# Optimization experiments

Measured on AMD Instinct MI355X. Metric: run time of the kernel, lower is better.

## Reference

```python
import jax, jax.numpy as jnp
import numpy as np

VOL = 64          # self.vol_size
SPACE = 0.2       # space_size (cubic), space_center = 0
IMG = 255.0       # normalization constant in the source (2*u/255 - 1)


def setup_inputs() -> dict:
    key = jax.random.key(0)
    ks = jax.random.split(key, 5)
    B, V, C, Hf, Wf = 2, 4, 32, 64, 64
    features = jax.random.normal(ks[0], (B, V, C, Hf, Wf), jnp.float32)
    # near-identity rotations, cameras ~0.5m away, focal ~200, principal point 128
    camera_R = jnp.eye(3, dtype=jnp.float32)[None, None] + 0.01 * jax.random.normal(ks[1], (B, V, 3, 3), jnp.float32)
    camera_T = jnp.array([0.0, 0.0, 0.5], jnp.float32) + 0.01 * jax.random.normal(ks[2], (B, V, 3), jnp.float32)
    K0 = jnp.array([[200.0, 0.0, 128.0], [0.0, 200.0, 128.0], [0.0, 0.0, 1.0]], jnp.float32)
    Kmask = jnp.array([[1.0, 0.0, 1.0], [0.0, 1.0, 1.0], [0.0, 0.0, 0.0]], jnp.float32)
    camera_K = K0[None, None] + 0.5 * jax.random.normal(ks[3], (B, V, 3, 3), jnp.float32) * Kmask
    root_world = 0.01 * jax.random.normal(ks[4], (B, 3), jnp.float32)
    return dict(features=features, camera_R=camera_R, camera_T=camera_T,
                camera_K=camera_K, root_world=root_world)


def _bilinear_sample(feat, x, y):
    """PyTorch F.grid_sample, mode=bilinear, padding=zeros, align_corners=False.
    feat: [N,C,H,W]; x,y: [N,P] pixel-space coords (already unnormalized).
    Returns [N,C,P]."""
    N, C, H, W = feat.shape
    x0 = jnp.floor(x); y0 = jnp.floor(y)
    x1 = x0 + 1.0;     y1 = y0 + 1.0
    wx1 = x - x0; wx0 = 1.0 - wx1
    wy1 = y - y0; wy0 = 1.0 - wy1
    feat_flat = feat.reshape(N, C, H * W)

    def gather(xi, yi, w):
        valid = (xi >= 0) & (xi <= W - 1) & (yi >= 0) & (yi <= H - 1)
        xi_c = jnp.clip(xi, 0, W - 1).astype(jnp.int32)
        yi_c = jnp.clip(yi, 0, H - 1).astype(jnp.int32)
        idx = yi_c * W + xi_c                                   # [N,P]
        vals = jnp.take_along_axis(feat_flat, idx[:, None, :], axis=2)  # [N,C,P]
        return vals * (w * valid.astype(feat.dtype))[:, None, :]

    return (gather(x0, y0, wx0 * wy0) + gather(x1, y0, wx1 * wy0)
            + gather(x0, y1, wx0 * wy1) + gather(x1, y1, wx1 * wy1))


def reference(features, camera_R, camera_T, camera_K, root_world):
    B, V, C, Hf, Wf = features.shape
    D = VOL
    # _build_grid: 64^3 points, xyz order, spanning SPACE around center 0
    r = jnp.arange(D, dtype=jnp.float32)
    z, y, x = jnp.meshgrid(r, r, r, indexing='ij')
    grid = jnp.stack([x, y, z], axis=0) / (D - 1)               # [3,D,D,D]
    pts = ((grid - 0.5) * SPACE).reshape(3, -1).T               # [P,3], P = D^3
    # relative camera translation: new_T = R @ root + T
    new_T = jnp.einsum('bvij,bj->bvi', camera_R, root_world) + camera_T
    # project: pts_cam = pts @ R^T + T  -> [B,V,P,3]
    pts_cam = jnp.einsum('pj,bvij->bvpi', pts, camera_R) + new_T[:, :, None, :]
    zc = jnp.maximum(pts_cam[..., 2], 1e-5)
    fx = camera_K[:, :, 0, 0][..., None]; fy = camera_K[:, :, 1, 1][..., None]
    cx = camera_K[:, :, 0, 2][..., None]; cy = camera_K[:, :, 1, 2][..., None]
    u = pts_cam[..., 0] * fx / zc + cx
    v = pts_cam[..., 1] * fy / zc + cy
    u_n = 2.0 * u / IMG - 1.0
    v_n = 2.0 * v / IMG - 1.0
    # unnormalize (align_corners=False): ix = ((g+1)*W - 1)/2
    px = ((u_n + 1.0) * Wf - 1.0) * 0.5
    py = ((v_n + 1.0) * Hf - 1.0) * 0.5
    feat_bv = features.reshape(B * V, C, Hf, Wf)
    vol = _bilinear_sample(feat_bv, px.reshape(B * V, -1), py.reshape(B * V, -1))  # [BV,C,P]
    vol = vol.reshape(B, V, C, D, D, D).mean(axis=1)            # average over views
    return vol
```

## Files before the change

kernel.cpp:

```cpp
#include <hip/hip_runtime.h>

#define B_   2
#define V_   4
#define C_   32
#define HW_  4096
#define D_   64
#define P_   (D_*D_*D_)
#define SCL_ (64.0f/255.0f)

#define TX_  16
#define TY_  8
#define TZ_  4
#define SLOTS_   96
#define SSTRIDE_ 80

typedef _Float16 half2v __attribute__((ext_vector_type(2)));
typedef __fp16  fp16x2 __attribute__((ext_vector_type(2)));

union Corner32 { uint4 u[2]; half2v h[8]; };
union H2U { half2v h; fp16x2 f; unsigned int u; };

__device__ __forceinline__ void project(const float* c, float X, float Y, float Z,
                                        float& px, float& py) {
    const float4 cA = *(const float4*)(c);
    const float4 cB = *(const float4*)(c + 4);
    const float4 cC = *(const float4*)(c + 8);
    const float4 cK = *(const float4*)(c + 12);
    const float xc = cA.x*X + cA.y*Y + cA.z*Z + cA.w;
    const float yc = cB.x*X + cB.y*Y + cB.z*Z + cB.w;
    float zc       = cC.x*X + cC.y*Y + cC.z*Z + cC.w;
    zc = fmaxf(zc, 1e-5f);
    const float inv = 1.0f / zc;
    px = (xc * inv) * cK.x + cK.z;
    py = (yc * inv) * cK.y + cK.w;
}

__global__ __launch_bounds__(256) void tx_kernel(const float* __restrict__ in,
                                                 unsigned int* __restrict__ out) {
    __shared__ float tile[32][65];
    const int bv  = blockIdx.x >> 6;
    const int hw0 = (blockIdx.x & 63) << 6;
    const int t   = threadIdx.x;
    const float* src = in + (size_t)bv * C_ * HW_ + hw0;
#pragma unroll
    for (int i = 0; i < 8; ++i) {
        int e = t + (i << 8);
        tile[e >> 6][e & 63] = src[(e >> 6) * HW_ + (e & 63)];
    }
    __syncthreads();
    unsigned int* dst = out + ((size_t)bv * HW_ + hw0) * (C_ / 2);
#pragma unroll
    for (int i = 0; i < 4; ++i) {
        int idx = t + (i << 8);
        int c  = (idx << 1) & 31;
        int hw = idx >> 4;
        half2v v = { (_Float16)tile[c][hw], (_Float16)tile[c + 1][hw] };
        dst[idx] = *(unsigned int*)&v;
    }
}

__global__ __launch_bounds__(256) void vol_kernel(
    const unsigned char* __restrict__ feat,
    const float* __restrict__ Rm,
    const float* __restrict__ Tm,
    const float* __restrict__ Km,
    const float* __restrict__ root,
    float* __restrict__ out)
{
    __shared__ __align__(16) float cam[4][20];
    __shared__ __align__(16) int rect4[4][4];
    __shared__ __align__(16) unsigned char sfeat[4][SLOTS_ * SSTRIDE_];

    const int t = threadIdx.x;
    const int b = blockIdx.x >> 9;
    const int tile = blockIdx.x & 511;
    const int gx0 = (tile & 3) * TX_;
    const int gy0 = ((tile >> 2) & 7) * TY_;
    const int gz0 = (tile >> 5) * TZ_;

    if (t < 4) {
        const int bv = b * V_ + t;
        const float* Rb = Rm + bv * 9;
        const float* Tb = Tm + bv * 3;
        const float* Kb = Km + bv * 9;
        const float rx = root[b*3+0], ry = root[b*3+1], rz = root[b*3+2];
        cam[t][0] = Rb[0]; cam[t][1] = Rb[1]; cam[t][2] = Rb[2];
        cam[t][3] = Rb[0]*rx + Rb[1]*ry + Rb[2]*rz + Tb[0];
        cam[t][4] = Rb[3]; cam[t][5] = Rb[4]; cam[t][6] = Rb[5];
        cam[t][7] = Rb[3]*rx + Rb[4]*ry + Rb[5]*rz + Tb[1];
        cam[t][8] = Rb[6]; cam[t][9] = Rb[7]; cam[t][10] = Rb[8];
        cam[t][11] = Rb[6]*rx + Rb[7]*ry + Rb[8]*rz + Tb[2];
        cam[t][12] = Kb[0] * SCL_;
        cam[t][13] = Kb[4] * SCL_;
        cam[t][14] = Kb[2] * SCL_ - 0.5f;
        cam[t][15] = Kb[5] * SCL_ - 0.5f;
    }
    __syncthreads();

    if (t < 32) {
        const int v = t & 3, c = t >> 2;
        const float X = ((float)(gx0 + (c & 1) * (TX_-1)) * (1.0f/63.0f) - 0.5f) * 0.2f;
        const float Y = ((float)(gy0 + ((c >> 1) & 1) * (TY_-1)) * (1.0f/63.0f) - 0.5f) * 0.2f;
        const float Z = ((float)(gz0 + (c >> 2) * (TZ_-1)) * (1.0f/63.0f) - 0.5f) * 0.2f;
        float px, py;
        project(&cam[v][0], X, Y, Z, px, py);
        float pxmn = px, pxmx = px, pymn = py, pymx = py;
#pragma unroll
        for (int m = 4; m <= 16; m <<= 1) {
            pxmn = fminf(pxmn, __shfl_xor(pxmn, m));
            pxmx = fmaxf(pxmx, __shfl_xor(pxmx, m));
            pymn = fminf(pymn, __shfl_xor(pymn, m));
            pymx = fmaxf(pymx, __shfl_xor(pymx, m));
        }
        if (t < 4) {
            int rx0 = (int)floorf(pxmn); rx0 = max(0, min(63, rx0));
            int rx1 = (int)floorf(pxmx) + 1; rx1 = max(rx0, min(63, rx1));
            int W = min(rx1 - rx0 + 1, 12);
            int ry0 = (int)floorf(pymn); ry0 = max(0, min(63, ry0));
            int ry1 = (int)floorf(pymx) + 1; ry1 = max(ry0, min(63, ry1));
            int H = min(ry1 - ry0 + 1, 8);
            rect4[t][0] = rx0; rect4[t][1] = ry0; rect4[t][2] = W; rect4[t][3] = H;
        }
    }
    __syncthreads();

    const int bvb = b * V_;
#pragma unroll
    for (int v = 0; v < 4; ++v) {
        const int rx0 = rect4[v][0], ry0 = rect4[v][1];
        const int W = rect4[v][2], H = rect4[v][3];
        const int nch = W * H * 4;
        const unsigned char* src = feat + (size_t)(bvb + v) * HW_ * 64;
        for (int s = t; s < nch; s += 256) {
            const int part = s & 3, pi = s >> 2;
            const int dy = pi / W, dx = pi - dy * W;
            const uint4 val = *(const uint4*)(src
                + (size_t)(((ry0 + dy) << 6) + rx0 + dx) * 64 + part * 16);
            *(uint4*)&sfeat[v][pi * SSTRIDE_ + part * 16] = val;
        }
    }
    __syncthreads();

    const int h = t & 1;
    const int vx = t >> 1;
    float Xk[4], Yk[4], Zk[4];
#pragma unroll
    for (int k = 0; k < 4; ++k) {
        const int local = vx + (k << 7);
        Xk[k] = ((float)(gx0 + (local & 15)) * (1.0f/63.0f) - 0.5f) * 0.2f;
        Yk[k] = ((float)(gy0 + ((local >> 4) & 7)) * (1.0f/63.0f) - 0.5f) * 0.2f;
        Zk[k] = ((float)(gz0 + (local >> 7)) * (1.0f/63.0f) - 0.5f) * 0.2f;
    }

    const half2v z2 = { (_Float16)0.0f, (_Float16)0.0f };
    half2v acc[4][8];
#pragma unroll
    for (int k = 0; k < 4; ++k)
#pragma unroll
        for (int j = 0; j < 8; ++j) acc[k][j] = z2;

#pragma unroll
    for (int v = 0; v < 4; ++v) {
        const float4 cA = *(const float4*)&cam[v][0];
        const float4 cB = *(const float4*)&cam[v][4];
        const float4 cC = *(const float4*)&cam[v][8];
        const float4 cK = *(const float4*)&cam[v][12];
        const int rx0 = rect4[v][0], ry0 = rect4[v][1], W = rect4[v][2];
        const unsigned char* vb = &sfeat[v][0] + (h << 5);
#pragma unroll
        for (int k = 0; k < 4; ++k) {
            const float xc = cA.x*Xk[k] + cA.y*Yk[k] + cA.z*Zk[k] + cA.w;
            const float yc = cB.x*Xk[k] + cB.y*Yk[k] + cB.z*Zk[k] + cB.w;
            float zc       = cC.x*Xk[k] + cC.y*Yk[k] + cC.z*Zk[k] + cC.w;
            zc = fmaxf(zc, 1e-5f);
            const float inv = 1.0f / zc;
            const float px = (xc * inv) * cK.x + cK.z;
            const float py = (yc * inv) * cK.y + cK.w;

            const float x0f = floorf(px), y0f = floorf(py);
            const float wx1 = px - x0f, wx0 = 1.0f - wx1;
            const float wy1 = py - y0f, wy0 = 1.0f - wy1;
            const float x1f = x0f + 1.0f, y1f = y0f + 1.0f;
            const float vx0 = (x0f >= 0.0f && x0f <= 63.0f) ? 0.25f : 0.0f;
            const float vx1 = (x1f >= 0.0f && x1f <= 63.0f) ? 0.25f : 0.0f;
            const float vy0 = (y0f >= 0.0f && y0f <= 63.0f) ? 1.0f : 0.0f;
            const float vy1 = (y1f >= 0.0f && y1f <= 63.0f) ? 1.0f : 0.0f;
            const float w00 = wx0*wy0*vx0*vy0, w01 = wx1*wy0*vx1*vy0;
            const float w10 = wx0*wy1*vx0*vy1, w11 = wx1*wy1*vx1*vy1;
            H2U u0, u1, u2, u3;
            u0.f = __builtin_amdgcn_cvt_pkrtz(w00, w00);
            u1.f = __builtin_amdgcn_cvt_pkrtz(w01, w01);
            u2.f = __builtin_amdgcn_cvt_pkrtz(w10, w10);
            u3.f = __builtin_amdgcn_cvt_pkrtz(w11, w11);

            const int x0c = (int)fminf(fmaxf(x0f, 0.0f), 63.0f);
            const int x1c = (int)fminf(fmaxf(x1f, 0.0f), 63.0f);
            const int y0c = (int)fminf(fmaxf(y0f, 0.0f), 63.0f);
            const int y1c = (int)fminf(fmaxf(y1f, 0.0f), 63.0f);
            const int dx0 = x0c - rx0, dx1 = x1c - rx0;
            const int r0 = (y0c - ry0) * W, r1 = (y1c - ry0) * W;
            const int o00 = (r0 + dx0) * SSTRIDE_, o01 = (r0 + dx1) * SSTRIDE_;
            const int o10 = (r1 + dx0) * SSTRIDE_, o11 = (r1 + dx1) * SSTRIDE_;

            Corner32 c00, c01, c10, c11;
            c00.u[0] = *(const uint4*)(vb + o00); c00.u[1] = *(const uint4*)(vb + o00 + 16);
            c01.u[0] = *(const uint4*)(vb + o01); c01.u[1] = *(const uint4*)(vb + o01 + 16);
            c10.u[0] = *(const uint4*)(vb + o10); c10.u[1] = *(const uint4*)(vb + o10 + 16);
            c11.u[0] = *(const uint4*)(vb + o11); c11.u[1] = *(const uint4*)(vb + o11 + 16);
#pragma unroll
            for (int j = 0; j < 8; ++j) {
                acc[k][j] += c00.h[j] * u0.h;
                acc[k][j] += c01.h[j] * u1.h;
                acc[k][j] += c10.h[j] * u2.h;
                acc[k][j] += c11.h[j] * u3.h;
            }
        }
    }

#pragma unroll
    for (int k = 0; k < 4; ++k) {
        const int local = vx + (k << 7);
        const int gx = gx0 + (local & 15);
        const int gy = gy0 + ((local >> 4) & 7);
        const int gz = gz0 + (local >> 7);
        const int p = (((gz << 6) + gy) << 6) + gx;
        float* ob = out + ((size_t)(b * C_) + (h << 4)) * P_ + p;
#pragma unroll
        for (int j = 0; j < 8; ++j) {
            __builtin_nontemporal_store((float)acc[k][j].x, ob + (size_t)(2*j  ) * P_);
            __builtin_nontemporal_store((float)acc[k][j].y, ob + (size_t)(2*j+1) * P_);
        }
    }
}

__global__ __launch_bounds__(256) void vol_fallback(
    const float* __restrict__ feat,
    const float* __restrict__ Rm, const float* __restrict__ Tm,
    const float* __restrict__ Km, const float* __restrict__ root,
    float* __restrict__ out)
{
    const int b = blockIdx.x >> 10;
    const int p = ((blockIdx.x & 1023) << 8) | threadIdx.x;
    const int xi = p & 63, yi = (p >> 6) & 63, zi = p >> 12;
    const float X = ((float)xi * (1.0f/63.0f) - 0.5f) * 0.2f;
    const float Y = ((float)yi * (1.0f/63.0f) - 0.5f) * 0.2f;
    const float Z = ((float)zi * (1.0f/63.0f) - 0.5f) * 0.2f;
    float acc[C_];
#pragma unroll
    for (int c = 0; c < C_; ++c) acc[c] = 0.0f;
    const float rx = root[b*3+0], ry = root[b*3+1], rz = root[b*3+2];
#pragma unroll
    for (int v = 0; v < V_; ++v) {
        const int bv = b * V_ + v;
        const float* Rb = Rm + bv * 9; const float* Tb = Tm + bv * 3;
        const float* Kb = Km + bv * 9;
        const float r00=Rb[0], r01=Rb[1], r02=Rb[2];
        const float r10=Rb[3], r11=Rb[4], r12=Rb[5];
        const float r20=Rb[6], r21=Rb[7], r22=Rb[8];
        const float t0 = r00*rx + r01*ry + r02*rz + Tb[0];
        const float t1 = r10*rx + r11*ry + r12*rz + Tb[1];
        const float t2 = r20*rx + r21*ry + r22*rz + Tb[2];
        const float xc = r00*X + r01*Y + r02*Z + t0;
        const float yc = r10*X + r11*Y + r12*Z + t1;
        float zc       = r20*X + r21*Y + r22*Z + t2;
        zc = fmaxf(zc, 1e-5f);
        const float inv = 1.0f / zc;
        const float px = xc * (Kb[0]*SCL_) * inv + (Kb[2]*SCL_ - 0.5f);
        const float py = yc * (Kb[4]*SCL_) * inv + (Kb[5]*SCL_ - 0.5f);
        const float x0f = floorf(px), y0f = floorf(py);
        const float wx1 = px - x0f, wx0 = 1.0f - wx1;
        const float wy1 = py - y0f, wy0 = 1.0f - wy1;
        const float x1f = x0f + 1.0f, y1f = y0f + 1.0f;
        const float vx0 = (x0f >= 0.0f && x0f <= 63.0f) ? 1.0f : 0.0f;
        const float vx1 = (x1f >= 0.0f && x1f <= 63.0f) ? 1.0f : 0.0f;
        const float vy0 = (y0f >= 0.0f && y0f <= 63.0f) ? 1.0f : 0.0f;
        const float vy1 = (y1f >= 0.0f && y1f <= 63.0f) ? 1.0f : 0.0f;
        const float w00 = wx0*wy0*vx0*vy0, w01 = wx1*wy0*vx1*vy0;
        const float w10 = wx0*wy1*vx0*vy1, w11 = wx1*wy1*vx1*vy1;
        const int x0c = (int)fminf(fmaxf(x0f, 0.0f), 63.0f);
        const int x1c = (int)fminf(fmaxf(x1f, 0.0f), 63.0f);
        const int y0c = (int)fminf(fmaxf(y0f, 0.0f), 63.0f);
        const int y1c = (int)fminf(fmaxf(y1f, 0.0f), 63.0f);
        const float* fb = feat + (size_t)bv * C_ * HW_;
        const int i00 = y0c*64 + x0c, i01 = y0c*64 + x1c;
        const int i10 = y1c*64 + x0c, i11 = y1c*64 + x1c;
#pragma unroll
        for (int c = 0; c < C_; ++c) {
            const float* f = fb + c * HW_;
            acc[c] += w00*f[i00] + w01*f[i01] + w10*f[i10] + w11*f[i11];
        }
    }
    float* ob = out + (size_t)b * C_ * P_ + p;
#pragma unroll
    for (int c = 0; c < C_; ++c) ob[(size_t)c * P_] = acc[c] * 0.25f;
}

extern "C" void kernel_launch(void* const* d_in, const int* in_sizes, int n_in,
                              void* d_out, int out_size, void* d_ws, size_t ws_size,
                              hipStream_t stream) {
    const float* feat = (const float*)d_in[0];
    const float* Rm   = (const float*)d_in[1];
    const float* Tm   = (const float*)d_in[2];
    const float* Km   = (const float*)d_in[3];
    const float* root = (const float*)d_in[4];
    float* out = (float*)d_out;

    const size_t need = (size_t)B_ * V_ * HW_ * C_ * sizeof(_Float16);
    if (ws_size >= need) {
        unsigned int* ftx = (unsigned int*)d_ws;
        tx_kernel<<<B_ * V_ * 64, 256, 0, stream>>>(feat, ftx);
        vol_kernel<<<B_ * 512, 256, 0, stream>>>(
            (const unsigned char*)ftx, Rm, Tm, Km, root, out);
    } else {
        vol_fallback<<<B_ * P_ / 256, 256, 0, stream>>>(feat, Rm, Tm, Km, root, out);
    }
}
```

Measured before the change: 96.74 us.

## Shrink voxel tiles to one voxel per thread and raise occupancy

Shrinks the vol_kernel block tile from 16x8x4 to 16x4x2 voxels, so each thread handles one voxel instead of four. The grid grows fourfold, the shared-memory feature footprint shrinks, and launch bounds request 6 blocks per CU. This aims to cut register pressure and raise occupancy to hide LDS and global latency. It also merges camera setup into the rect-computing warp to drop one barrier, and replaces the strided gather loop and integer divide with a single-pass load using a reciprocal multiply. In exchange, the per-block setup, bounding-box projection and staging are repeated four times as often, and neighbouring blocks reload more overlapping feature data.

```diff
diff --git a/kernel.cpp b/kernel.cpp
--- a/kernel.cpp
+++ b/kernel.cpp
@@ -8,10 +8,12 @@
 #define P_   (D_*D_*D_)
 #define SCL_ (64.0f/255.0f)
 
-#define TX_  16
-#define TY_  8
-#define TZ_  4
-#define SLOTS_   96
+#define TXv_ 16
+#define TYv_ 4
+#define TZv_ 2
+#define WCAP_ 10
+#define HCAP_ 6
+#define SLOTS_   64
 #define SSTRIDE_ 80
 
 typedef _Float16 half2v __attribute__((ext_vector_type(2)));
@@ -19,21 +21,6 @@
 
 union Corner32 { uint4 u[2]; half2v h[8]; };
 union H2U { half2v h; fp16x2 f; unsigned int u; };
-
-__device__ __forceinline__ void project(const float* c, float X, float Y, float Z,
-                                        float& px, float& py) {
-    const float4 cA = *(const float4*)(c);
-    const float4 cB = *(const float4*)(c + 4);
-    const float4 cC = *(const float4*)(c + 8);
-    const float4 cK = *(const float4*)(c + 12);
-    const float xc = cA.x*X + cA.y*Y + cA.z*Z + cA.w;
-    const float yc = cB.x*X + cB.y*Y + cB.z*Z + cB.w;
-    float zc       = cC.x*X + cC.y*Y + cC.z*Z + cC.w;
-    zc = fmaxf(zc, 1e-5f);
-    const float inv = 1.0f / zc;
-    px = (xc * inv) * cK.x + cK.z;
-    py = (yc * inv) * cK.y + cK.w;
-}
 
 __global__ __launch_bounds__(256) void tx_kernel(const float* __restrict__ in,
                                                  unsigned int* __restrict__ out) {
@@ -59,7 +46,7 @@
     }
 }
 
-__global__ __launch_bounds__(256) void vol_kernel(
+__global__ __launch_bounds__(256, 6) void vol_kernel(
     const unsigned char* __restrict__ feat,
     const float* __restrict__ Rm,
     const float* __restrict__ Tm,
@@ -68,42 +55,43 @@
     float* __restrict__ out)
 {
     __shared__ __align__(16) float cam[4][20];
-    __shared__ __align__(16) int rect4[4][4];
+    __shared__ __align__(16) int   srect[4][8];
     __shared__ __align__(16) unsigned char sfeat[4][SLOTS_ * SSTRIDE_];
 
     const int t = threadIdx.x;
-    const int b = blockIdx.x >> 9;
-    const int tile = blockIdx.x & 511;
-    const int gx0 = (tile & 3) * TX_;
-    const int gy0 = ((tile >> 2) & 7) * TY_;
-    const int gz0 = (tile >> 5) * TZ_;
-
-    if (t < 4) {
-        const int bv = b * V_ + t;
+    const int b = blockIdx.x >> 11;
+    const int tile = blockIdx.x & 2047;
+    const int gx0 = (tile & 3) << 4;
+    const int gy0 = ((tile >> 2) & 15) << 2;
+    const int gz0 = (tile >> 6) << 1;
+
+    if (t < 32) {
+        const int v = t & 3, c = t >> 2;
+        const int bv = b * V_ + v;
         const float* Rb = Rm + bv * 9;
         const float* Tb = Tm + bv * 3;
         const float* Kb = Km + bv * 9;
         const float rx = root[b*3+0], ry = root[b*3+1], rz = root[b*3+2];
-        cam[t][0] = Rb[0]; cam[t][1] = Rb[1]; cam[t][2] = Rb[2];
-        cam[t][3] = Rb[0]*rx + Rb[1]*ry + Rb[2]*rz + Tb[0];
-        cam[t][4] = Rb[3]; cam[t][5] = Rb[4]; cam[t][6] = Rb[5];
-        cam[t][7] = Rb[3]*rx + Rb[4]*ry + Rb[5]*rz + Tb[1];
-        cam[t][8] = Rb[6]; cam[t][9] = Rb[7]; cam[t][10] = Rb[8];
-        cam[t][11] = Rb[6]*rx + Rb[7]*ry + Rb[8]*rz + Tb[2];
-        cam[t][12] = Kb[0] * SCL_;
-        cam[t][13] = Kb[4] * SCL_;
-        cam[t][14] = Kb[2] * SCL_ - 0.5f;
-        cam[t][15] = Kb[5] * SCL_ - 0.5f;
-    }
-    __syncthreads();
-
-    if (t < 32) {
-        const int v = t & 3, c = t >> 2;
-        const float X = ((float)(gx0 + (c & 1) * (TX_-1)) * (1.0f/63.0f) - 0.5f) * 0.2f;
-        const float Y = ((float)(gy0 + ((c >> 1) & 1) * (TY_-1)) * (1.0f/63.0f) - 0.5f) * 0.2f;
-        const float Z = ((float)(gz0 + (c >> 2) * (TZ_-1)) * (1.0f/63.0f) - 0.5f) * 0.2f;
-        float px, py;
-        project(&cam[v][0], X, Y, Z, px, py);
+        const float r00=Rb[0], r01=Rb[1], r02=Rb[2];
+        const float r10=Rb[3], r11=Rb[4], r12=Rb[5];
+        const float r20=Rb[6], r21=Rb[7], r22=Rb[8];
+        const float t0 = r00*rx + r01*ry + r02*rz + Tb[0];
+        const float t1 = r10*rx + r11*ry + r12*rz + Tb[1];
+        const float t2 = r20*rx + r21*ry + r22*rz + Tb[2];
+        const float fx = Kb[0] * SCL_, fy = Kb[4] * SCL_;
+        const float cx = Kb[2] * SCL_ - 0.5f, cy = Kb[5] * SCL_ - 0.5f;
+
+        const float X = ((float)(gx0 + (c & 1) * (TXv_-1)) * (1.0f/63.0f) - 0.5f) * 0.2f;
+        const float Y = ((float)(gy0 + ((c >> 1) & 1) * (TYv_-1)) * (1.0f/63.0f) - 0.5f) * 0.2f;
+        const float Z = ((float)(gz0 + (c >> 2) * (TZv_-1)) * (1.0f/63.0f) - 0.5f) * 0.2f;
+        const float xc = r00*X + r01*Y + r02*Z + t0;
+        const float yc = r10*X + r11*Y + r12*Z + t1;
+        float zc       = r20*X + r21*Y + r22*Z + t2;
+        zc = fmaxf(zc, 1e-5f);
+        const float inv = 1.0f / zc;
+        float px = (xc * inv) * fx + cx;
+        float py = (yc * inv) * fy + cy;
+
         float pxmn = px, pxmx = px, pymn = py, pymx = py;
 #pragma unroll
         for (int m = 4; m <= 16; m <<= 1) {
@@ -112,14 +100,20 @@
             pymn = fminf(pymn, __shfl_xor(pymn, m));
             pymx = fmaxf(pymx, __shfl_xor(pymx, m));
         }
-        if (t < 4) {
+        if (c == 0) {
+            cam[v][0] = r00; cam[v][1] = r01; cam[v][2] = r02; cam[v][3] = t0;
+            cam[v][4] = r10; cam[v][5] = r11; cam[v][6] = r12; cam[v][7] = t1;
+            cam[v][8] = r20; cam[v][9] = r21; cam[v][10] = r22; cam[v][11] = t2;
+            cam[v][12] = fx; cam[v][13] = fy; cam[v][14] = cx; cam[v][15] = cy;
             int rx0 = (int)floorf(pxmn); rx0 = max(0, min(63, rx0));
             int rx1 = (int)floorf(pxmx) + 1; rx1 = max(rx0, min(63, rx1));
-            int W = min(rx1 - rx0 + 1, 12);
+            const int W = min(rx1 - rx0 + 1, WCAP_);
             int ry0 = (int)floorf(pymn); ry0 = max(0, min(63, ry0));
             int ry1 = (int)floorf(pymx) + 1; ry1 = max(ry0, min(63, ry1));
-            int H = min(ry1 - ry0 + 1, 8);
-            rect4[t][0] = rx0; rect4[t][1] = ry0; rect4[t][2] = W; rect4[t][3] = H;
+            const int H = min(ry1 - ry0 + 1, HCAP_);
+            srect[v][0] = rx0; srect[v][1] = ry0; srect[v][2] = W; srect[v][3] = H;
+            srect[v][4] = 65536 / W + 1;
+            srect[v][5] = W * H * 4;
         }
     }
     __syncthreads();
@@ -127,13 +121,14 @@
     const int bvb = b * V_;
 #pragma unroll
     for (int v = 0; v < 4; ++v) {
-        const int rx0 = rect4[v][0], ry0 = rect4[v][1];
-        const int W = rect4[v][2], H = rect4[v][3];
-        const int nch = W * H * 4;
-        const unsigned char* src = feat + (size_t)(bvb + v) * HW_ * 64;
-        for (int s = t; s < nch; s += 256) {
-            const int part = s & 3, pi = s >> 2;
-            const int dy = pi / W, dx = pi - dy * W;
+        const int nch = srect[v][5];
+        if (t < nch) {
+            const int rx0 = srect[v][0], ry0 = srect[v][1];
+            const int W = srect[v][2], M = srect[v][4];
+            const int part = t & 3, pi = t >> 2;
+            const int dy = (pi * M) >> 16;
+            const int dx = pi - dy * W;
+            const unsigned char* src = feat + (size_t)(bvb + v) * HW_ * 64;
             const uint4 val = *(const uint4*)(src
                 + (size_t)(((ry0 + dy) << 6) + rx0 + dx) * 64 + part * 16);
             *(uint4*)&sfeat[v][pi * SSTRIDE_ + part * 16] = val;
@@ -143,21 +138,14 @@
 
     const int h = t & 1;
     const int vx = t >> 1;
-    float Xk[4], Yk[4], Zk[4];
-#pragma unroll
-    for (int k = 0; k < 4; ++k) {
-        const int local = vx + (k << 7);
-        Xk[k] = ((float)(gx0 + (local & 15)) * (1.0f/63.0f) - 0.5f) * 0.2f;
-        Yk[k] = ((float)(gy0 + ((local >> 4) & 7)) * (1.0f/63.0f) - 0.5f) * 0.2f;
-        Zk[k] = ((float)(gz0 + (local >> 7)) * (1.0f/63.0f) - 0.5f) * 0.2f;
-    }
+    const float X = ((float)(gx0 + (vx & 15)) * (1.0f/63.0f) - 0.5f) * 0.2f;
+    const float Y = ((float)(gy0 + ((vx >> 4) & 3)) * (1.0f/63.0f) - 0.5f) * 0.2f;
+    const float Z = ((float)(gz0 + (vx >> 6)) * (1.0f/63.0f) - 0.5f) * 0.2f;
 
     const half2v z2 = { (_Float16)0.0f, (_Float16)0.0f };
-    half2v acc[4][8];
-#pragma unroll
-    for (int k = 0; k < 4; ++k)
-#pragma unroll
-        for (int j = 0; j < 8; ++j) acc[k][j] = z2;
+    half2v acc[8];
+#pragma unroll
+    for (int j = 0; j < 8; ++j) acc[j] = z2;
 
 #pragma unroll
     for (int v = 0; v < 4; ++v) {
@@ -165,71 +153,65 @@
         const float4 cB = *(const float4*)&cam[v][4];
         const float4 cC = *(const float4*)&cam[v][8];
         const float4 cK = *(const float4*)&cam[v][12];
-        const int rx0 = rect4[v][0], ry0 = rect4[v][1], W = rect4[v][2];
+        const int rx0 = srect[v][0], ry0 = srect[v][1], W = srect[v][2];
+
+        const float xc = cA.x*X + cA.y*Y + cA.z*Z + cA.w;
+        const float yc = cB.x*X + cB.y*Y + cB.z*Z + cB.w;
+        float zc       = cC.x*X + cC.y*Y + cC.z*Z + cC.w;
+        zc = fmaxf(zc, 1e-5f);
+        const float inv = 1.0f / zc;
+        const float px = (xc * inv) * cK.x + cK.z;
+        const float py = (yc * inv) * cK.y + cK.w;
+
+        const float x0f = floorf(px), y0f = floorf(py);
+        const float wx1 = px - x0f, wx0 = 1.0f - wx1;
+        const float wy1 = py - y0f, wy0 = 1.0f - wy1;
+        const float x1f = x0f + 1.0f, y1f = y0f + 1.0f;
+        const float vx0 = (x0f >= 0.0f && x0f <= 63.0f) ? 0.25f : 0.0f;
+        const float vx1 = (x1f >= 0.0f && x1f <= 63.0f) ? 0.25f : 0.0f;
+        const float vy0 = (y0f >= 0.0f && y0f <= 63.0f) ? 1.0f : 0.0f;
+        const float vy1 = (y1f >= 0.0f && y1f <= 63.0f) ? 1.0f : 0.0f;
+        const float w00 = wx0*wy0*vx0*vy0, w01 = wx1*wy0*vx1*vy0;
+        const float w10 = wx0*wy1*vx0*vy1, w11 = wx1*wy1*vx1*vy1;
+        H2U u0, u1, u2, u3;
+        u0.f = __builtin_amdgcn_cvt_pkrtz(w00, w00);
+        u1.f = __builtin_amdgcn_cvt_pkrtz(w01, w01);
+        u2.f = __builtin_amdgcn_cvt_pkrtz(w10, w10);
+        u3.f = __builtin_amdgcn_cvt_pkrtz(w11, w11);
+
+        const int x0c = (int)fminf(fmaxf(x0f, 0.0f), 63.0f);
+        const int x1c = (int)fminf(fmaxf(x1f, 0.0f), 63.0f);
+        const int y0c = (int)fminf(fmaxf(y0f, 0.0f), 63.0f);
+        const int y1c = (int)fminf(fmaxf(y1f, 0.0f), 63.0f);
+        const int dx0 = x0c - rx0, dx1 = x1c - rx0;
+        const int r0 = (y0c - ry0) * W, r1 = (y1c - ry0) * W;
+        const int o00 = (r0 + dx0) * SSTRIDE_, o01 = (r0 + dx1) * SSTRIDE_;
+        const int o10 = (r1 + dx0) * SSTRIDE_, o11 = (r1 + dx1) * SSTRIDE_;
+
         const unsigned char* vb = &sfeat[v][0] + (h << 5);
-#pragma unroll
-        for (int k = 0; k < 4; ++k) {
-            const float xc = cA.x*Xk[k] + cA.y*Yk[k] + cA.z*Zk[k] + cA.w;
-            const float yc = cB.x*Xk[k] + cB.y*Yk[k] + cB.z*Zk[k] + cB.w;
-            float zc       = cC.x*Xk[k] + cC.y*Yk[k] + cC.z*Zk[k] + cC.w;
-            zc = fmaxf(zc, 1e-5f);
-            const float inv = 1.0f / zc;
-            const float px = (xc * inv) * cK.x + cK.z;
-            const float py = (yc * inv) * cK.y + cK.w;
-
-            const float x0f = floorf(px), y0f = floorf(py);
-            const float wx1 = px - x0f, wx0 = 1.0f - wx1;
-            const float wy1 = py - y0f, wy0 = 1.0f - wy1;
-            const float x1f = x0f + 1.0f, y1f = y0f + 1.0f;
-            const float vx0 = (x0f >= 0.0f && x0f <= 63.0f) ? 0.25f : 0.0f;
-            const float vx1 = (x1f >= 0.0f && x1f <= 63.0f) ? 0.25f : 0.0f;
-            const float vy0 = (y0f >= 0.0f && y0f <= 63.0f) ? 1.0f : 0.0f;
-            const float vy1 = (y1f >= 0.0f && y1f <= 63.0f) ? 1.0f : 0.0f;
-            const float w00 = wx0*wy0*vx0*vy0, w01 = wx1*wy0*vx1*vy0;
-            const float w10 = wx0*wy1*vx0*vy1, w11 = wx1*wy1*vx1*vy1;
-            H2U u0, u1, u2, u3;
-            u0.f = __builtin_amdgcn_cvt_pkrtz(w00, w00);
-            u1.f = __builtin_amdgcn_cvt_pkrtz(w01, w01);
-            u2.f = __builtin_amdgcn_cvt_pkrtz(w10, w10);
-            u3.f = __builtin_amdgcn_cvt_pkrtz(w11, w11);
-
-            const int x0c = (int)fminf(fmaxf(x0f, 0.0f), 63.0f);
-            const int x1c = (int)fminf(fmaxf(x1f, 0.0f), 63.0f);
-            const int y0c = (int)fminf(fmaxf(y0f, 0.0f), 63.0f);
-            const int y1c = (int)fminf(fmaxf(y1f, 0.0f), 63.0f);
-            const int dx0 = x0c - rx0, dx1 = x1c - rx0;
-            const int r0 = (y0c - ry0) * W, r1 = (y1c - ry0) * W;
-            const int o00 = (r0 + dx0) * SSTRIDE_, o01 = (r0 + dx1) * SSTRIDE_;
-            const int o10 = (r1 + dx0) * SSTRIDE_, o11 = (r1 + dx1) * SSTRIDE_;
-
-            Corner32 c00, c01, c10, c11;
-            c00.u[0] = *(const uint4*)(vb + o00); c00.u[1] = *(const uint4*)(vb + o00 + 16);
-            c01.u[0] = *(const uint4*)(vb + o01); c01.u[1] = *(const uint4*)(vb + o01 + 16);
-            c10.u[0] = *(const uint4*)(vb + o10); c10.u[1] = *(const uint4*)(vb + o10 + 16);
-            c11.u[0] = *(const uint4*)(vb + o11); c11.u[1] = *(const uint4*)(vb + o11 + 16);
-#pragma unroll
-            for (int j = 0; j < 8; ++j) {
-                acc[k][j] += c00.h[j] * u0.h;
-                acc[k][j] += c01.h[j] * u1.h;
-                acc[k][j] += c10.h[j] * u2.h;
-                acc[k][j] += c11.h[j] * u3.h;
-            }
-        }
-    }
-
-#pragma unroll
-    for (int k = 0; k < 4; ++k) {
-        const int local = vx + (k << 7);
-        const int gx = gx0 + (local & 15);
-        const int gy = gy0 + ((local >> 4) & 7);
-        const int gz = gz0 + (local >> 7);
-        const int p = (((gz << 6) + gy) << 6) + gx;
-        float* ob = out + ((size_t)(b * C_) + (h << 4)) * P_ + p;
+        Corner32 c00, c01, c10, c11;
+        c00.u[0] = *(const uint4*)(vb + o00); c00.u[1] = *(const uint4*)(vb + o00 + 16);
+        c01.u[0] = *(const uint4*)(vb + o01); c01.u[1] = *(const uint4*)(vb + o01 + 16);
+        c10.u[0] = *(const uint4*)(vb + o10); c10.u[1] = *(const uint4*)(vb + o10 + 16);
+        c11.u[0] = *(const uint4*)(vb + o11); c11.u[1] = *(const uint4*)(vb + o11 + 16);
 #pragma unroll
         for (int j = 0; j < 8; ++j) {
-            __builtin_nontemporal_store((float)acc[k][j].x, ob + (size_t)(2*j  ) * P_);
-            __builtin_nontemporal_store((float)acc[k][j].y, ob + (size_t)(2*j+1) * P_);
-        }
+            acc[j] += c00.h[j] * u0.h;
+            acc[j] += c01.h[j] * u1.h;
+            acc[j] += c10.h[j] * u2.h;
+            acc[j] += c11.h[j] * u3.h;
+        }
+    }
+
+    const int gx = gx0 + (vx & 15);
+    const int gy = gy0 + ((vx >> 4) & 3);
+    const int gz = gz0 + (vx >> 6);
+    const int p = (((gz << 6) + gy) << 6) + gx;
+    float* ob = out + ((size_t)(b * C_) + (h << 4)) * P_ + p;
+#pragma unroll
+    for (int j = 0; j < 8; ++j) {
+        __builtin_nontemporal_store((float)acc[j].x, ob + (size_t)(2*j  ) * P_);
+        __builtin_nontemporal_store((float)acc[j].y, ob + (size_t)(2*j+1) * P_);
     }
 }
 
@@ -309,7 +291,7 @@
     if (ws_size >= need) {
         unsigned int* ftx = (unsigned int*)d_ws;
         tx_kernel<<<B_ * V_ * 64, 256, 0, stream>>>(feat, ftx);
-        vol_kernel<<<B_ * 512, 256, 0, stream>>>(
+        vol_kernel<<<B_ * 2048, 256, 0, stream>>>(
             (const unsigned char*)ftx, Rm, Tm, Km, root, out);
     } else {
         vol_fallback<<<B_ * P_ / 256, 256, 0, stream>>>(feat, Rm, Tm, Km, root, out);
```

Result: no change. 96.45 us (-0.3%).
